# Optimization experiments

Hardware: AMD Instinct MI355X
Metric: run time of the kernel (lower is better)

The kernel has to match this reference:

```python
import jax, jax.numpy as jnp
import numpy as np
from jax import lax

EPS = 1e-5
TRUNK_C, REG_C, GPOOL_C = 256, 192, 64
B, H, W = 256, 19, 19


def setup_inputs() -> dict:
    key = jax.random.key(0)
    ks = jax.random.split(key, 18)
    def bn_params(k, c):
        k1, k2, k3, k4 = jax.random.split(k, 4)
        return (jax.random.normal(k1, (c,)) * 0.1 + 1.0,   # gamma
                jax.random.normal(k2, (c,)) * 0.1,          # beta
                jax.random.normal(k3, (c,)) * 0.1,          # running mean
                jax.random.uniform(k4, (c,)) * 0.5 + 0.5)   # running var
    bn1_g, bn1_b, bn1_m, bn1_v = bn_params(ks[0], TRUNK_C)
    bn1b_g, bn1b_b, bn1b_m, bn1b_v = bn_params(ks[1], GPOOL_C)
    bn2_g, bn2_b, bn2_m, bn2_v = bn_params(ks[2], REG_C)
    x = jax.random.normal(ks[3], (B, TRUNK_C, H, W), dtype=jnp.float32)
    w1a = jax.random.normal(ks[4], (REG_C, TRUNK_C, 3, 3), dtype=jnp.float32) * (1.0 / np.sqrt(TRUNK_C * 9))
    w1b = jax.random.normal(ks[5], (GPOOL_C, TRUNK_C, 3, 3), dtype=jnp.float32) * (1.0 / np.sqrt(TRUNK_C * 9))
    w_lin = jax.random.normal(ks[6], (REG_C, 3 * GPOOL_C), dtype=jnp.float32) * (1.0 / np.sqrt(3 * GPOOL_C))
    w2 = jax.random.normal(ks[7], (TRUNK_C, REG_C, 3, 3), dtype=jnp.float32) * (1.0 / np.sqrt(REG_C * 9))
    return {
        'x': x, 'bn1_g': bn1_g, 'bn1_b': bn1_b, 'bn1_m': bn1_m, 'bn1_v': bn1_v,
        'w1a': w1a, 'w1b': w1b,
        'bn1b_g': bn1b_g, 'bn1b_b': bn1b_b, 'bn1b_m': bn1b_m, 'bn1b_v': bn1b_v,
        'w_lin': w_lin,
        'bn2_g': bn2_g, 'bn2_b': bn2_b, 'bn2_m': bn2_m, 'bn2_v': bn2_v,
        'w2': w2,
    }


def _bn(x, g, b, m, v):
    # inference batchnorm over channel dim of NCHW
    inv = g / jnp.sqrt(v + EPS)
    return (x - m[:, None, None]) * inv[:, None, None] + b[:, None, None]


def _mish(x):
    return x * jnp.tanh(jax.nn.softplus(x))


def _conv(x, w):
    return lax.conv_general_dilated(x, w, (1, 1), 'SAME',
                                    dimension_numbers=('NCHW', 'OIHW', 'NCHW'))


def _kata_gpool(x):
    # x: [B, C, H, W] -> [B, 3C]: mean, mean*(sqrt(N)-14)/10, max
    b, c, h, w = x.shape
    n = float(h * w)
    sqrt_n = n ** 0.5
    mean = jnp.sum(x, axis=(2, 3)) / n
    max_val = jnp.max(x, axis=(2, 3))
    scaled_mean = mean * ((sqrt_n - 14.0) / 10.0)
    return jnp.concatenate([mean, scaled_mean, max_val], axis=1)


def reference(x, bn1_g, bn1_b, bn1_m, bn1_v, w1a, w1b,
              bn1b_g, bn1b_b, bn1b_m, bn1b_v, w_lin,
              bn2_g, bn2_b, bn2_m, bn2_v, w2):
    out = _mish(_bn(x, bn1_g, bn1_b, bn1_m, bn1_v))
    reg = _conv(out, w1a)                       # [B, REG_C, H, W]
    gp = _conv(out, w1b)                        # [B, GPOOL_C, H, W]
    gp = _mish(_bn(gp, bn1b_g, bn1b_b, bn1b_m, bn1b_v))
    gp_pooled = _kata_gpool(gp)                 # [B, 3*GPOOL_C]
    gp_out = gp_pooled @ w_lin.T                # [B, REG_C]
    reg = reg + gp_out[:, :, None, None]
    out2 = _mish(_bn(reg, bn2_g, bn2_b, bn2_m, bn2_v))
    out2 = _conv(out2, w2)
    return out2 + x
```

## Files before the change

kernel.cpp:

```cpp
#include <hip/hip_runtime.h>
#include <hip/hip_bf16.h>
#include <math.h>


#define BATCH   256
#define TRUNK_C 256
#define REG_C   192
#define GPOOL_C 64
#define HH      19
#define WW      19
#define HW      361
#define PP      441
#define EPS     1e-5f

typedef __hip_bfloat16 bf16;
typedef __attribute__((ext_vector_type(8))) short short8;
typedef __attribute__((ext_vector_type(4))) float floatx4;

__device__ __forceinline__ float b2f(bf16 v) { return __bfloat162float(v); }
__device__ __forceinline__ bf16  f2b(float v) { return __float2bfloat16(v); }

__device__ __forceinline__ float mish_f(float v) {
    if (v > 20.0f) return v;
    float u = __expf(v);
    float n = u * (u + 2.0f);
    return v * __fdividef(n, n + 2.0f);
}

__device__ __forceinline__ void gload_lds16(const void* gsrc, void* lds) {
    __builtin_amdgcn_global_load_lds(
        (const __attribute__((address_space(1))) void*)gsrc,
        (__attribute__((address_space(3))) void*)lds, 16, 0, 0);
}

__global__ void prep_bn_kernel(const float* g1, const float* b1, const float* m1, const float* v1,
                               const float* g1b, const float* b1b, const float* m1b, const float* v1b,
                               const float* g2, const float* b2, const float* m2, const float* v2,
                               float* bnbuf) {
    int t = threadIdx.x;
    if (t < 256) {
        float s = g1[t] / sqrtf(v1[t] + EPS);
        bnbuf[t] = s;
        bnbuf[256 + t] = b1[t] - m1[t] * s;
    } else if (t < 320) {
        int c = t - 256;
        float s = g1b[c] / sqrtf(v1b[c] + EPS);
        bnbuf[512 + c] = s;
        bnbuf[576 + c] = b1b[c] - m1b[c] * s;
    } else if (t < 512) {
        int c = t - 320;
        float s = g2[c] / sqrtf(v2[c] + EPS);
        bnbuf[640 + c] = s;
        bnbuf[832 + c] = b2[c] - m2[c] * s;
    }
}

__global__ void prep_w_kernel(const float* __restrict__ w1a, const float* __restrict__ w1b,
                              const float* __restrict__ w2,
                              bf16* __restrict__ w1c_p, bf16* __restrict__ w2_p) {
    const int T1 = 16 * 72 * 64 * 8;
    const int T2 = 16 * 54 * 64 * 8;
    for (int i = blockIdx.x * blockDim.x + threadIdx.x; i < T1 + T2;
         i += gridDim.x * blockDim.x) {
        if (i < T1) {
            int j = i & 7, lane = (i >> 3) & 63;
            int kc = (i >> 9) % 72, cog = (i >> 9) / 72;
            int co = cog * 16 + (lane & 15);
            int k = kc * 32 + ((lane >> 4) << 3) + j;
            int r = k >> 8, ci = k & 255;
            float v = (co < 192) ? w1a[co * 2304 + ci * 9 + r]
                                 : w1b[(co - 192) * 2304 + ci * 9 + r];
            w1c_p[i] = f2b(v);
        } else {
            int i2 = i - T1;
            int j = i2 & 7, lane = (i2 >> 3) & 63;
            int kc = (i2 >> 9) % 54, cog = (i2 >> 9) / 54;
            int co = cog * 16 + (lane & 15);
            int k = kc * 32 + ((lane >> 4) << 3) + j;
            int r = k / 192, ci = k % 192;
            w2_p[i2] = f2b(w2[co * 1728 + ci * 9 + r]);
        }
    }
}

__global__ void zero_border_kernel(bf16* __restrict__ act_pad, bf16* __restrict__ reg_pad) {
    int b = blockIdx.x;
    int t = threadIdx.x;
    for (int pp = 0; pp < PP; ++pp) {
        int r = pp / 21, c = pp % 21;
        bool border = (r == 0) | (r == 20) | (c == 0) | (c == 20);
        if (!border) continue;
        act_pad[((size_t)b * PP + pp) * TRUNK_C + t] = f2b(0.0f);
        if (t < REG_C) reg_pad[((size_t)b * PP + pp) * REG_C + t] = f2b(0.0f);
    }
}

__global__ __launch_bounds__(256)
void bn1_mish_t_kernel(const float* __restrict__ x, const float* __restrict__ bnbuf,
                       bf16* __restrict__ act_pad) {
    __shared__ float lds[256][32];
    int pc = blockIdx.x;
    int b  = blockIdx.y;
    int t  = threadIdx.x;
    int p0 = pc * 32;
    int px = t & 31;
#pragma unroll
    for (int it = 0; it < 32; ++it) {
        int ci = it * 8 + (t >> 5);
        int p  = p0 + px;
        float v = 0.0f;
        if (p < HW) v = x[((size_t)b * TRUNK_C + ci) * HW + p];
        v = v * bnbuf[ci] + bnbuf[256 + ci];
        lds[ci][px ^ (ci >> 3)] = mish_f(v);
    }
    __syncthreads();
#pragma unroll
    for (int it = 0; it < 4; ++it) {
        int pl = it * 8 + (t >> 5);
        int p  = p0 + pl;
        if (p >= HW) continue;
        int ch = t & 31;
        short8 vv;
#pragma unroll
        for (int j = 0; j < 8; ++j) {
            bf16 h = f2b(lds[ch * 8 + j][pl ^ ch]);
            short s;
            __builtin_memcpy(&s, &h, 2);
            vv[j] = s;
        }
        int pp = (p / WW + 1) * 21 + (p % WW + 1);
        *(short8*)(act_pad + ((size_t)b * PP + pp) * TRUNK_C + ch * 8) = vv;
    }
}

__global__ __launch_bounds__(512)
void conv1_kernel(const bf16* __restrict__ act,
                  const bf16* __restrict__ wfrag,
                  bf16* __restrict__ reg_out,
                  bf16* __restrict__ gp_out,
                  const float* __restrict__ ep_scale, const float* __restrict__ ep_bias) {
    const int CIN = 256, NKC = 72;
    __shared__ __align__(16) bf16 atile[3][128 * 32];
    const int b   = blockIdx.x;
    const int mt  = blockIdx.y;
    const int t   = threadIdx.x;
    const int w   = t >> 6, lane = t & 63;
    const int mi  = w >> 2, ni = w & 3;
    const int l15 = lane & 15, quad = lane >> 4;

    int spxl = t >> 2;
    int sq   = t & 3;
    int ss   = sq ^ ((spxl >> 1) & 3);
    int sp   = mt * 128 + spxl; if (sp > 360) sp = 360;
    const bf16* sbase = act + ((size_t)b * PP + (sp / WW) * 21 + (sp % WW)) * CIN + (ss << 3);

    const bf16* wb[4];
#pragma unroll
    for (int ns = 0; ns < 4; ++ns)
        wb[ns] = wfrag + ((size_t)(ni * 4 + ns) * NKC * 64 + lane) * 8;

    int aoff[4];
#pragma unroll
    for (int ms = 0; ms < 4; ++ms) {
        int row = mi * 64 + ms * 16 + l15;
        aoff[ms] = row * 32 + ((quad ^ ((row >> 1) & 3)) << 3);
    }

    auto stage = [&](int buf, int kc) {
        int r = kc >> 3, c = kc & 7;
        int off = ((r / 3) * 21 + (r % 3)) * CIN + (c << 5);
        gload_lds16(sbase + off, &atile[buf][w << 9]);
    };

    floatx4 acc[4][4];
#pragma unroll
    for (int i = 0; i < 4; ++i)
#pragma unroll
        for (int j = 0; j < 4; ++j) acc[i][j] = (floatx4){0.f, 0.f, 0.f, 0.f};

    short8 afr[4], bfrA[4], bfrB[4];
    stage(0, 0);
    stage(1, 1);
#pragma unroll
    for (int ns = 0; ns < 4; ++ns) bfrA[ns] = *(const short8*)(wb[ns]);

    for (int kc = 0; kc < NKC; kc += 2) {
        asm volatile("s_waitcnt vmcnt(5)" ::: "memory");
        __builtin_amdgcn_sched_barrier(0);
        __builtin_amdgcn_s_barrier();
        __builtin_amdgcn_sched_barrier(0);
        {
            int s1 = kc + 2; if (s1 > NKC - 1) s1 = NKC - 1;
            stage((kc + 2) % 3, s1);
        }
#pragma unroll
        for (int ns = 0; ns < 4; ++ns)
            bfrB[ns] = *(const short8*)(wb[ns] + (size_t)(kc + 1) * 512);
        {
            const bf16* at = atile[kc % 3];
#pragma unroll
            for (int ms = 0; ms < 4; ++ms)
                afr[ms] = *(const short8*)(at + aoff[ms]);
        }
#pragma unroll
        for (int ms = 0; ms < 4; ++ms)
#pragma unroll
            for (int ns = 0; ns < 4; ++ns)
                acc[ms][ns] = __builtin_amdgcn_mfma_f32_16x16x32_bf16(
                    afr[ms], bfrA[ns], acc[ms][ns], 0, 0, 0);

        asm volatile("s_waitcnt vmcnt(5)" ::: "memory");
        __builtin_amdgcn_sched_barrier(0);
        __builtin_amdgcn_s_barrier();
        __builtin_amdgcn_sched_barrier(0);
        {
            int s2 = kc + 3; if (s2 > NKC - 1) s2 = NKC - 1;
            stage((kc + 3) % 3, s2);
        }
        {
            int nb = kc + 2; if (nb > NKC - 1) nb = NKC - 1;
#pragma unroll
            for (int ns = 0; ns < 4; ++ns)
                bfrA[ns] = *(const short8*)(wb[ns] + (size_t)nb * 512);
        }
        {
            const bf16* at = atile[(kc + 1) % 3];
#pragma unroll
            for (int ms = 0; ms < 4; ++ms)
                afr[ms] = *(const short8*)(at + aoff[ms]);
        }
#pragma unroll
        for (int ms = 0; ms < 4; ++ms)
#pragma unroll
            for (int ns = 0; ns < 4; ++ns)
                acc[ms][ns] = __builtin_amdgcn_mfma_f32_16x16x32_bf16(
                    afr[ms], bfrB[ns], acc[ms][ns], 0, 0, 0);
    }

    float scl[4], bia[4];
#pragma unroll
    for (int ns = 0; ns < 4; ++ns) {
        int co = (ni * 4 + ns) * 16 + l15;
        if (co >= 192) { scl[ns] = ep_scale[co - 192]; bia[ns] = ep_bias[co - 192]; }
    }
#pragma unroll
    for (int ms = 0; ms < 4; ++ms) {
#pragma unroll
        for (int rg = 0; rg < 4; ++rg) {
            int p = mt * 128 + mi * 64 + ms * 16 + quad * 4 + rg;
            if (p > 360) continue;
            size_t ppad = (size_t)b * PP + (p / WW + 1) * 21 + (p % WW + 1);
#pragma unroll
            for (int ns = 0; ns < 4; ++ns) {
                int co = (ni * 4 + ns) * 16 + l15;
                float v = acc[ms][ns][rg];
                if (co < 192) {
                    reg_out[ppad * REG_C + co] = f2b(v);
                } else {
                    v = mish_f(v * scl[ns] + bia[ns]);
                    gp_out[((size_t)b * HW + p) * GPOOL_C + (co - 192)] = f2b(v);
                }
            }
        }
    }
}

__global__ __launch_bounds__(512)
void conv2_kernel(const bf16* __restrict__ act,
                  const bf16* __restrict__ wfrag,
                  const float* __restrict__ resid,
                  float* __restrict__ out) {
    const int CIN = 192, NKC = 54;
    __shared__ __align__(16) bf16 atile[3][128 * 32];
    const int b   = blockIdx.x;
    const int mt  = blockIdx.y;
    const int t   = threadIdx.x;
    const int w   = t >> 6, lane = t & 63;
    const int pw  = w >> 2, cw = w & 3;
    const int l15 = lane & 15, quad = lane >> 4;

    int spxl = t >> 2;
    int sq   = t & 3;
    int ss   = sq ^ ((spxl >> 1) & 3);
    int sp   = mt * 128 + spxl; if (sp > 360) sp = 360;
    const bf16* sbase = act + ((size_t)b * PP + (sp / WW) * 21 + (sp % WW)) * CIN + (ss << 3);

    const bf16* wb[4];
#pragma unroll
    for (int ms = 0; ms < 4; ++ms)
        wb[ms] = wfrag + ((size_t)(cw * 4 + ms) * NKC * 64 + lane) * 8;

    int aoff[4];
#pragma unroll
    for (int ns = 0; ns < 4; ++ns) {
        int row = pw * 64 + ns * 16 + l15;
        aoff[ns] = row * 32 + ((quad ^ ((row >> 1) & 3)) << 3);
    }

    auto stage = [&](int buf, int kc) {
        int r = kc / 6, c = kc % 6;
        int off = ((r / 3) * 21 + (r % 3)) * CIN + (c << 5);
        gload_lds16(sbase + off, &atile[buf][w << 9]);
    };

    floatx4 acc[4][4];
#pragma unroll
    for (int i = 0; i < 4; ++i)
#pragma unroll
        for (int j = 0; j < 4; ++j) acc[i][j] = (floatx4){0.f, 0.f, 0.f, 0.f};

    short8 bfa[4], wfrA[4], wfrB[4];
    stage(0, 0);
    stage(1, 1);
#pragma unroll
    for (int ms = 0; ms < 4; ++ms) wfrA[ms] = *(const short8*)(wb[ms]);

    for (int kc = 0; kc < NKC; kc += 2) {
        asm volatile("s_waitcnt vmcnt(5)" ::: "memory");
        __builtin_amdgcn_sched_barrier(0);
        __builtin_amdgcn_s_barrier();
        __builtin_amdgcn_sched_barrier(0);
        {
            int s1 = kc + 2; if (s1 > NKC - 1) s1 = NKC - 1;
            stage((kc + 2) % 3, s1);
        }
#pragma unroll
        for (int ms = 0; ms < 4; ++ms)
            wfrB[ms] = *(const short8*)(wb[ms] + (size_t)(kc + 1) * 512);
        {
            const bf16* at = atile[kc % 3];
#pragma unroll
            for (int ns = 0; ns < 4; ++ns)
                bfa[ns] = *(const short8*)(at + aoff[ns]);
        }
#pragma unroll
        for (int ms = 0; ms < 4; ++ms)
#pragma unroll
            for (int ns = 0; ns < 4; ++ns)
                acc[ms][ns] = __builtin_amdgcn_mfma_f32_16x16x32_bf16(
                    wfrA[ms], bfa[ns], acc[ms][ns], 0, 0, 0);

        asm volatile("s_waitcnt vmcnt(5)" ::: "memory");
        __builtin_amdgcn_sched_barrier(0);
        __builtin_amdgcn_s_barrier();
        __builtin_amdgcn_sched_barrier(0);
        {
            int s2 = kc + 3; if (s2 > NKC - 1) s2 = NKC - 1;
            stage((kc + 3) % 3, s2);
        }
        {
            int nb = kc + 2; if (nb > NKC - 1) nb = NKC - 1;
#pragma unroll
            for (int ms = 0; ms < 4; ++ms)
                wfrA[ms] = *(const short8*)(wb[ms] + (size_t)nb * 512);
        }
        {
            const bf16* at = atile[(kc + 1) % 3];
#pragma unroll
            for (int ns = 0; ns < 4; ++ns)
                bfa[ns] = *(const short8*)(at + aoff[ns]);
        }
#pragma unroll
        for (int ms = 0; ms < 4; ++ms)
#pragma unroll
            for (int ns = 0; ns < 4; ++ns)
                acc[ms][ns] = __builtin_amdgcn_mfma_f32_16x16x32_bf16(
                    wfrB[ms], bfa[ns], acc[ms][ns], 0, 0, 0);
    }

#pragma unroll
    for (int ns = 0; ns < 4; ++ns) {
        int p = mt * 128 + pw * 64 + ns * 16 + l15;
        if (p > 360) continue;
#pragma unroll
        for (int ms = 0; ms < 4; ++ms) {
#pragma unroll
            for (int rg = 0; rg < 4; ++rg) {
                int co = (cw * 4 + ms) * 16 + quad * 4 + rg;
                size_t idx = ((size_t)b * TRUNK_C + co) * HW + p;
                out[idx] = acc[ms][ns][rg] + resid[idx];
            }
        }
    }
}

__global__ void gpool_lin_kernel(const bf16* __restrict__ gp, const float* __restrict__ w_lin,
                                 float* __restrict__ gpout) {
    __shared__ float ls[4][64], lm[4][64];
    __shared__ float pooled_s[192];
    int b = blockIdx.x;
    int t = threadIdx.x;
    int c = t & 63, sub = t >> 6;
    float s = 0.0f, mx = -1e30f;
    for (int p = sub; p < HW; p += 4) {
        float v = b2f(gp[((size_t)b * HW + p) * GPOOL_C + c]);
        s += v;
        mx = fmaxf(mx, v);
    }
    ls[sub][c] = s; lm[sub][c] = mx;
    __syncthreads();
    if (t < 64) {
        float ss = ls[0][t] + ls[1][t] + ls[2][t] + ls[3][t];
        float mm = fmaxf(fmaxf(lm[0][t], lm[1][t]), fmaxf(lm[2][t], lm[3][t]));
        float mean = ss * (1.0f / 361.0f);
        pooled_s[t] = mean;
        pooled_s[64 + t] = mean * 0.5f;
        pooled_s[128 + t] = mm;
    }
    __syncthreads();
    if (t < 192) {
        const float4* wr4 = (const float4*)(w_lin + t * 192);
        float acc = 0.0f;
#pragma unroll 8
        for (int j = 0; j < 48; ++j) {
            float4 wv = wr4[j];
            acc = fmaf(pooled_s[j * 4 + 0], wv.x, acc);
            acc = fmaf(pooled_s[j * 4 + 1], wv.y, acc);
            acc = fmaf(pooled_s[j * 4 + 2], wv.z, acc);
            acc = fmaf(pooled_s[j * 4 + 3], wv.w, acc);
        }
        gpout[b * 192 + t] = acc;
    }
}

__global__ __launch_bounds__(256)
void add_bn2_mish_kernel(bf16* __restrict__ reg_pad, const float* __restrict__ gpout,
                         const float* __restrict__ bnbuf) {
    const int total = BATCH * HW * 24;
    int i = blockIdx.x * blockDim.x + threadIdx.x;
    if (i >= total) return;
    int g  = i % 24;
    int bp = i / 24;
    int p  = bp % HW;
    int b  = bp / HW;
    int pp = (p / WW + 1) * 21 + (p % WW + 1);
    size_t idx = ((size_t)b * PP + pp) * REG_C + g * 8;
    short8 v = *(const short8*)(reg_pad + idx);
    const float* gpo = gpout + b * 192 + g * 8;
    const float* sc  = bnbuf + 640 + g * 8;
    const float* bi  = bnbuf + 832 + g * 8;
    short8 o;
#pragma unroll
    for (int j = 0; j < 8; ++j) {
        short sj = v[j];
        bf16 h;
        __builtin_memcpy(&h, &sj, 2);
        float f = b2f(h) + gpo[j];
        f = f * sc[j] + bi[j];
        h = f2b(mish_f(f));
        __builtin_memcpy(&sj, &h, 2);
        o[j] = sj;
    }
    *(short8*)(reg_pad + idx) = o;
}

extern "C" void kernel_launch(void* const* d_in, const int* in_sizes, int n_in,
                              void* d_out, int out_size, void* d_ws, size_t ws_size,
                              hipStream_t stream) {
    const float* x     = (const float*)d_in[0];
    const float* bn1_g = (const float*)d_in[1];
    const float* bn1_b = (const float*)d_in[2];
    const float* bn1_m = (const float*)d_in[3];
    const float* bn1_v = (const float*)d_in[4];
    const float* w1a   = (const float*)d_in[5];
    const float* w1b   = (const float*)d_in[6];
    const float* bn1b_g = (const float*)d_in[7];
    const float* bn1b_b = (const float*)d_in[8];
    const float* bn1b_m = (const float*)d_in[9];
    const float* bn1b_v = (const float*)d_in[10];
    const float* w_lin  = (const float*)d_in[11];
    const float* bn2_g  = (const float*)d_in[12];
    const float* bn2_b  = (const float*)d_in[13];
    const float* bn2_m  = (const float*)d_in[14];
    const float* bn2_v  = (const float*)d_in[15];
    const float* w2     = (const float*)d_in[16];
    float* out = (float*)d_out;

    char* ws = (char*)d_ws;
    size_t off = 0;
    auto alloc = [&](size_t bytes) {
        void* p = ws + off;
        off += (bytes + 255) & ~(size_t)255;
        return p;
    };
    bf16*  act_pad = (bf16*)alloc((size_t)BATCH * PP * TRUNK_C * sizeof(bf16));
    bf16*  reg_pad = (bf16*)alloc((size_t)BATCH * PP * REG_C * sizeof(bf16));
    bf16*  gp      = (bf16*)alloc((size_t)BATCH * HW * GPOOL_C * sizeof(bf16));
    bf16*  w1c_p   = (bf16*)alloc((size_t)16 * 72 * 64 * 8 * sizeof(bf16));
    bf16*  w2_p    = (bf16*)alloc((size_t)16 * 54 * 64 * 8 * sizeof(bf16));
    float* gpout   = (float*)alloc((size_t)BATCH * 192 * sizeof(float));
    float* bnbuf   = (float*)alloc(1024 * sizeof(float));
    (void)ws_size;

    hipLaunchKernelGGL(prep_bn_kernel, dim3(1), dim3(512), 0, stream,
                       bn1_g, bn1_b, bn1_m, bn1_v,
                       bn1b_g, bn1b_b, bn1b_m, bn1b_v,
                       bn2_g, bn2_b, bn2_m, bn2_v, bnbuf);
    hipLaunchKernelGGL(prep_w_kernel, dim3(1024), dim3(256), 0, stream,
                       w1a, w1b, w2, w1c_p, w2_p);
    hipLaunchKernelGGL(zero_border_kernel, dim3(BATCH), dim3(256), 0, stream,
                       act_pad, reg_pad);

    hipLaunchKernelGGL(bn1_mish_t_kernel, dim3(12, BATCH), dim3(256), 0, stream,
                       x, bnbuf, act_pad);

    hipLaunchKernelGGL(conv1_kernel, dim3(BATCH, 3), dim3(512), 0, stream,
                       act_pad, w1c_p, reg_pad, gp, bnbuf + 512, bnbuf + 576);

    hipLaunchKernelGGL(gpool_lin_kernel, dim3(BATCH), dim3(256), 0, stream,
                       gp, w_lin, gpout);

    {
        int total = BATCH * HW * 24;
        hipLaunchKernelGGL(add_bn2_mish_kernel, dim3((total + 255) / 256), dim3(256), 0, stream,
                           reg_pad, gpout, bnbuf);
    }

    hipLaunchKernelGGL(conv2_kernel, dim3(BATCH, 3), dim3(512), 0, stream,
                       reg_pad, w2_p, x, out);
}
```

Before: 680.8 us.

## Split conv output channels across grid z, deepen LDS pipeline, merge prep kernels

Both conv kernels now use 256-thread blocks with a third grid dimension that splits output channels in two, so each block computes half the channels for its 128-pixel tile. The LDS A-tile ring grows from three to four buffers and is staged one iteration further ahead, with adjusted vmcnt waits. The three setup kernels (BN folding, weight packing, border zeroing) are merged into one flat launch, and border zeroing becomes vectorized. This adds more concurrent blocks and deeper latency hiding, at the cost of loading each activation tile twice, once per channel half.

```diff
diff --git a/kernel.cpp b/kernel.cpp
--- a/kernel.cpp
+++ b/kernel.cpp
@@ -33,35 +33,23 @@
         (__attribute__((address_space(3))) void*)lds, 16, 0, 0);
 }
 
-__global__ void prep_bn_kernel(const float* g1, const float* b1, const float* m1, const float* v1,
-                               const float* g1b, const float* b1b, const float* m1b, const float* v1b,
-                               const float* g2, const float* b2, const float* m2, const float* v2,
-                               float* bnbuf) {
-    int t = threadIdx.x;
-    if (t < 256) {
-        float s = g1[t] / sqrtf(v1[t] + EPS);
-        bnbuf[t] = s;
-        bnbuf[256 + t] = b1[t] - m1[t] * s;
-    } else if (t < 320) {
-        int c = t - 256;
-        float s = g1b[c] / sqrtf(v1b[c] + EPS);
-        bnbuf[512 + c] = s;
-        bnbuf[576 + c] = b1b[c] - m1b[c] * s;
-    } else if (t < 512) {
-        int c = t - 320;
-        float s = g2[c] / sqrtf(v2[c] + EPS);
-        bnbuf[640 + c] = s;
-        bnbuf[832 + c] = b2[c] - m2[c] * s;
-    }
-}
-
-__global__ void prep_w_kernel(const float* __restrict__ w1a, const float* __restrict__ w1b,
-                              const float* __restrict__ w2,
-                              bf16* __restrict__ w1c_p, bf16* __restrict__ w2_p) {
-    const int T1 = 16 * 72 * 64 * 8;
-    const int T2 = 16 * 54 * 64 * 8;
-    for (int i = blockIdx.x * blockDim.x + threadIdx.x; i < T1 + T2;
-         i += gridDim.x * blockDim.x) {
+__global__ void prep_kernel(
+    const float* g1, const float* b1, const float* m1, const float* v1,
+    const float* g1b, const float* b1b, const float* m1b, const float* v1b,
+    const float* g2, const float* b2, const float* m2, const float* v2,
+    const float* __restrict__ w1a, const float* __restrict__ w1b,
+    const float* __restrict__ w2,
+    bf16* __restrict__ w1c_p, bf16* __restrict__ w2_p,
+    bf16* __restrict__ act_pad, bf16* __restrict__ reg_pad,
+    float* bnbuf)
+{
+    const int T1  = 16 * 72 * 64 * 8;
+    const int T2  = 16 * 54 * 64 * 8;
+    const int TW  = T1 + T2;
+    const int TBa = BATCH * 80 * 32;
+    const int TBr = BATCH * 80 * 24;
+    int i = blockIdx.x * blockDim.x + threadIdx.x;
+    if (i < TW) {
         if (i < T1) {
             int j = i & 7, lane = (i >> 3) & 63;
             int kc = (i >> 9) % 72, cog = (i >> 9) / 72;
@@ -80,18 +68,39 @@
             int r = k / 192, ci = k % 192;
             w2_p[i2] = f2b(w2[co * 1728 + ci * 9 + r]);
         }
-    }
-}
-
-__global__ void zero_border_kernel(bf16* __restrict__ act_pad, bf16* __restrict__ reg_pad) {
-    int b = blockIdx.x;
-    int t = threadIdx.x;
-    for (int pp = 0; pp < PP; ++pp) {
-        int r = pp / 21, c = pp % 21;
-        bool border = (r == 0) | (r == 20) | (c == 0) | (c == 20);
-        if (!border) continue;
-        act_pad[((size_t)b * PP + pp) * TRUNK_C + t] = f2b(0.0f);
-        if (t < REG_C) reg_pad[((size_t)b * PP + pp) * REG_C + t] = f2b(0.0f);
+    } else if (i < TW + TBa + TBr) {
+        int j = i - TW;
+        bool isact = j < TBa;
+        if (!isact) j -= TBa;
+        int nb = isact ? 32 : 24;
+        int b = j / (80 * nb);
+        int rem = j - b * (80 * nb);
+        int e = rem / nb, g = rem - (rem / nb) * nb;
+        int pp;
+        if (e < 21) pp = e;
+        else if (e < 42) pp = 420 + (e - 21);
+        else if (e < 61) pp = (e - 41) * 21;
+        else pp = (e - 60) * 21 + 20;
+        short8 z = {0, 0, 0, 0, 0, 0, 0, 0};
+        if (isact) *(short8*)(act_pad + ((size_t)b * PP + pp) * TRUNK_C + g * 8) = z;
+        else       *(short8*)(reg_pad + ((size_t)b * PP + pp) * REG_C + g * 8) = z;
+    } else {
+        int t = i - (TW + TBa + TBr);
+        if (t < 256) {
+            float s = g1[t] / sqrtf(v1[t] + EPS);
+            bnbuf[t] = s;
+            bnbuf[256 + t] = b1[t] - m1[t] * s;
+        } else if (t < 320) {
+            int c = t - 256;
+            float s = g1b[c] / sqrtf(v1b[c] + EPS);
+            bnbuf[512 + c] = s;
+            bnbuf[576 + c] = b1b[c] - m1b[c] * s;
+        } else if (t < 512) {
+            int c = t - 320;
+            float s = g2[c] / sqrtf(v2[c] + EPS);
+            bnbuf[640 + c] = s;
+            bnbuf[832 + c] = b2[c] - m2[c] * s;
+        }
     }
 }
 
@@ -133,31 +142,34 @@
     }
 }
 
-__global__ __launch_bounds__(512)
+__global__ __launch_bounds__(256, 3)
 void conv1_kernel(const bf16* __restrict__ act,
                   const bf16* __restrict__ wfrag,
                   bf16* __restrict__ reg_out,
                   bf16* __restrict__ gp_out,
                   const float* __restrict__ ep_scale, const float* __restrict__ ep_bias) {
     const int CIN = 256, NKC = 72;
-    __shared__ __align__(16) bf16 atile[3][128 * 32];
+    __shared__ __align__(16) bf16 atile[4][128 * 32];
     const int b   = blockIdx.x;
     const int mt  = blockIdx.y;
+    const int nh  = blockIdx.z;
     const int t   = threadIdx.x;
     const int w   = t >> 6, lane = t & 63;
-    const int mi  = w >> 2, ni = w & 3;
+    const int mi  = w >> 1, ni = w & 1;
     const int l15 = lane & 15, quad = lane >> 4;
 
-    int spxl = t >> 2;
+    int row0 = t >> 2;
     int sq   = t & 3;
-    int ss   = sq ^ ((spxl >> 1) & 3);
-    int sp   = mt * 128 + spxl; if (sp > 360) sp = 360;
-    const bf16* sbase = act + ((size_t)b * PP + (sp / WW) * 21 + (sp % WW)) * CIN + (ss << 3);
+    int ss   = sq ^ ((row0 >> 1) & 3);
+    int sp0  = mt * 128 + row0;      if (sp0 > 360) sp0 = 360;
+    int sp1  = mt * 128 + row0 + 64; if (sp1 > 360) sp1 = 360;
+    const bf16* sb0 = act + ((size_t)b * PP + (sp0 / WW) * 21 + (sp0 % WW)) * CIN + (ss << 3);
+    const bf16* sb1 = act + ((size_t)b * PP + (sp1 / WW) * 21 + (sp1 % WW)) * CIN + (ss << 3);
 
     const bf16* wb[4];
 #pragma unroll
     for (int ns = 0; ns < 4; ++ns)
-        wb[ns] = wfrag + ((size_t)(ni * 4 + ns) * NKC * 64 + lane) * 8;
+        wb[ns] = wfrag + ((size_t)(nh * 8 + ni * 4 + ns) * NKC * 64 + lane) * 8;
 
     int aoff[4];
 #pragma unroll
@@ -169,7 +181,9 @@
     auto stage = [&](int buf, int kc) {
         int r = kc >> 3, c = kc & 7;
         int off = ((r / 3) * 21 + (r % 3)) * CIN + (c << 5);
-        gload_lds16(sbase + off, &atile[buf][w << 9]);
+        bf16* dst = &atile[buf][w << 9];
+        gload_lds16(sb0 + off, dst);
+        gload_lds16(sb1 + off, dst + 2048);
     };
 
     floatx4 acc[4][4];
@@ -181,23 +195,28 @@
     short8 afr[4], bfrA[4], bfrB[4];
     stage(0, 0);
     stage(1, 1);
+    asm volatile("" ::: "memory");
 #pragma unroll
     for (int ns = 0; ns < 4; ++ns) bfrA[ns] = *(const short8*)(wb[ns]);
+    asm volatile("" ::: "memory");
+    stage(2, 2);
 
     for (int kc = 0; kc < NKC; kc += 2) {
-        asm volatile("s_waitcnt vmcnt(5)" ::: "memory");
+        if (kc == 0) asm volatile("s_waitcnt vmcnt(8)" ::: "memory");
+        else         asm volatile("s_waitcnt vmcnt(12)" ::: "memory");
         __builtin_amdgcn_sched_barrier(0);
         __builtin_amdgcn_s_barrier();
         __builtin_amdgcn_sched_barrier(0);
-        {
-            int s1 = kc + 2; if (s1 > NKC - 1) s1 = NKC - 1;
-            stage((kc + 2) % 3, s1);
-        }
 #pragma unroll
         for (int ns = 0; ns < 4; ++ns)
             bfrB[ns] = *(const short8*)(wb[ns] + (size_t)(kc + 1) * 512);
-        {
-            const bf16* at = atile[kc % 3];
+        asm volatile("" ::: "memory");
+        {
+            int s = kc + 3; if (s > NKC - 1) s = NKC - 1;
+            stage((kc + 3) & 3, s);
+        }
+        {
+            const bf16* at = atile[kc & 3];
 #pragma unroll
             for (int ms = 0; ms < 4; ++ms)
                 afr[ms] = *(const short8*)(at + aoff[ms]);
@@ -209,22 +228,23 @@
                 acc[ms][ns] = __builtin_amdgcn_mfma_f32_16x16x32_bf16(
                     afr[ms], bfrA[ns], acc[ms][ns], 0, 0, 0);
 
-        asm volatile("s_waitcnt vmcnt(5)" ::: "memory");
+        asm volatile("s_waitcnt vmcnt(12)" ::: "memory");
         __builtin_amdgcn_sched_barrier(0);
         __builtin_amdgcn_s_barrier();
         __builtin_amdgcn_sched_barrier(0);
         {
-            int s2 = kc + 3; if (s2 > NKC - 1) s2 = NKC - 1;
-            stage((kc + 3) % 3, s2);
-        }
-        {
             int nb = kc + 2; if (nb > NKC - 1) nb = NKC - 1;
 #pragma unroll
             for (int ns = 0; ns < 4; ++ns)
                 bfrA[ns] = *(const short8*)(wb[ns] + (size_t)nb * 512);
         }
-        {
-            const bf16* at = atile[(kc + 1) % 3];
+        asm volatile("" ::: "memory");
+        {
+            int s = kc + 4; if (s > NKC - 1) s = NKC - 1;
+            stage((kc + 4) & 3, s);
+        }
+        {
+            const bf16* at = atile[(kc + 1) & 3];
 #pragma unroll
             for (int ms = 0; ms < 4; ++ms)
                 afr[ms] = *(const short8*)(at + aoff[ms]);
@@ -240,7 +260,7 @@
     float scl[4], bia[4];
 #pragma unroll
     for (int ns = 0; ns < 4; ++ns) {
-        int co = (ni * 4 + ns) * 16 + l15;
+        int co = (nh * 8 + ni * 4 + ns) * 16 + l15;
         if (co >= 192) { scl[ns] = ep_scale[co - 192]; bia[ns] = ep_bias[co - 192]; }
     }
 #pragma unroll
@@ -252,7 +272,7 @@
             size_t ppad = (size_t)b * PP + (p / WW + 1) * 21 + (p % WW + 1);
 #pragma unroll
             for (int ns = 0; ns < 4; ++ns) {
-                int co = (ni * 4 + ns) * 16 + l15;
+                int co = (nh * 8 + ni * 4 + ns) * 16 + l15;
                 float v = acc[ms][ns][rg];
                 if (co < 192) {
                     reg_out[ppad * REG_C + co] = f2b(v);
@@ -265,30 +285,33 @@
     }
 }
 
-__global__ __launch_bounds__(512)
+__global__ __launch_bounds__(256, 3)
 void conv2_kernel(const bf16* __restrict__ act,
                   const bf16* __restrict__ wfrag,
                   const float* __restrict__ resid,
                   float* __restrict__ out) {
     const int CIN = 192, NKC = 54;
-    __shared__ __align__(16) bf16 atile[3][128 * 32];
+    __shared__ __align__(16) bf16 atile[4][128 * 32];
     const int b   = blockIdx.x;
     const int mt  = blockIdx.y;
+    const int nh  = blockIdx.z;
     const int t   = threadIdx.x;
     const int w   = t >> 6, lane = t & 63;
-    const int pw  = w >> 2, cw = w & 3;
+    const int pw  = w >> 1, cw = w & 1;
     const int l15 = lane & 15, quad = lane >> 4;
 
-    int spxl = t >> 2;
+    int row0 = t >> 2;
     int sq   = t & 3;
-    int ss   = sq ^ ((spxl >> 1) & 3);
-    int sp   = mt * 128 + spxl; if (sp > 360) sp = 360;
-    const bf16* sbase = act + ((size_t)b * PP + (sp / WW) * 21 + (sp % WW)) * CIN + (ss << 3);
+    int ss   = sq ^ ((row0 >> 1) & 3);
+    int sp0  = mt * 128 + row0;      if (sp0 > 360) sp0 = 360;
+    int sp1  = mt * 128 + row0 + 64; if (sp1 > 360) sp1 = 360;
+    const bf16* sb0 = act + ((size_t)b * PP + (sp0 / WW) * 21 + (sp0 % WW)) * CIN + (ss << 3);
+    const bf16* sb1 = act + ((size_t)b * PP + (sp1 / WW) * 21 + (sp1 % WW)) * CIN + (ss << 3);
 
     const bf16* wb[4];
 #pragma unroll
     for (int ms = 0; ms < 4; ++ms)
-        wb[ms] = wfrag + ((size_t)(cw * 4 + ms) * NKC * 64 + lane) * 8;
+        wb[ms] = wfrag + ((size_t)(nh * 8 + cw * 4 + ms) * NKC * 64 + lane) * 8;
 
     int aoff[4];
 #pragma unroll
@@ -300,7 +323,9 @@
     auto stage = [&](int buf, int kc) {
         int r = kc / 6, c = kc % 6;
         int off = ((r / 3) * 21 + (r % 3)) * CIN + (c << 5);
-        gload_lds16(sbase + off, &atile[buf][w << 9]);
+        bf16* dst = &atile[buf][w << 9];
+        gload_lds16(sb0 + off, dst);
+        gload_lds16(sb1 + off, dst + 2048);
     };
 
     floatx4 acc[4][4];
@@ -312,23 +337,28 @@
     short8 bfa[4], wfrA[4], wfrB[4];
     stage(0, 0);
     stage(1, 1);
+    asm volatile("" ::: "memory");
 #pragma unroll
     for (int ms = 0; ms < 4; ++ms) wfrA[ms] = *(const short8*)(wb[ms]);
+    asm volatile("" ::: "memory");
+    stage(2, 2);
 
     for (int kc = 0; kc < NKC; kc += 2) {
-        asm volatile("s_waitcnt vmcnt(5)" ::: "memory");
+        if (kc == 0) asm volatile("s_waitcnt vmcnt(8)" ::: "memory");
+        else         asm volatile("s_waitcnt vmcnt(12)" ::: "memory");
         __builtin_amdgcn_sched_barrier(0);
         __builtin_amdgcn_s_barrier();
         __builtin_amdgcn_sched_barrier(0);
-        {
-            int s1 = kc + 2; if (s1 > NKC - 1) s1 = NKC - 1;
-            stage((kc + 2) % 3, s1);
-        }
 #pragma unroll
         for (int ms = 0; ms < 4; ++ms)
             wfrB[ms] = *(const short8*)(wb[ms] + (size_t)(kc + 1) * 512);
-        {
-            const bf16* at = atile[kc % 3];
+        asm volatile("" ::: "memory");
+        {
+            int s = kc + 3; if (s > NKC - 1) s = NKC - 1;
+            stage((kc + 3) & 3, s);
+        }
+        {
+            const bf16* at = atile[kc & 3];
 #pragma unroll
             for (int ns = 0; ns < 4; ++ns)
                 bfa[ns] = *(const short8*)(at + aoff[ns]);
@@ -340,22 +370,23 @@
                 acc[ms][ns] = __builtin_amdgcn_mfma_f32_16x16x32_bf16(
                     wfrA[ms], bfa[ns], acc[ms][ns], 0, 0, 0);
 
-        asm volatile("s_waitcnt vmcnt(5)" ::: "memory");
+        asm volatile("s_waitcnt vmcnt(12)" ::: "memory");
         __builtin_amdgcn_sched_barrier(0);
         __builtin_amdgcn_s_barrier();
         __builtin_amdgcn_sched_barrier(0);
-        {
-            int s2 = kc + 3; if (s2 > NKC - 1) s2 = NKC - 1;
-            stage((kc + 3) % 3, s2);
-        }
         {
             int nb = kc + 2; if (nb > NKC - 1) nb = NKC - 1;
 #pragma unroll
             for (int ms = 0; ms < 4; ++ms)
                 wfrA[ms] = *(const short8*)(wb[ms] + (size_t)nb * 512);
         }
-        {
-            const bf16* at = atile[(kc + 1) % 3];
+        asm volatile("" ::: "memory");
+        {
+            int s = kc + 4; if (s > NKC - 1) s = NKC - 1;
+            stage((kc + 4) & 3, s);
+        }
+        {
+            const bf16* at = atile[(kc + 1) & 3];
 #pragma unroll
             for (int ns = 0; ns < 4; ++ns)
                 bfa[ns] = *(const short8*)(at + aoff[ns]);
@@ -376,7 +407,7 @@
         for (int ms = 0; ms < 4; ++ms) {
 #pragma unroll
             for (int rg = 0; rg < 4; ++rg) {
-                int co = (cw * 4 + ms) * 16 + quad * 4 + rg;
+                int co = (nh * 8 + cw * 4 + ms) * 16 + quad * 4 + rg;
                 size_t idx = ((size_t)b * TRUNK_C + co) * HW + p;
                 out[idx] = acc[ms][ns][rg] + resid[idx];
             }
@@ -492,19 +523,20 @@
     float* bnbuf   = (float*)alloc(1024 * sizeof(float));
     (void)ws_size;
 
-    hipLaunchKernelGGL(prep_bn_kernel, dim3(1), dim3(512), 0, stream,
-                       bn1_g, bn1_b, bn1_m, bn1_v,
-                       bn1b_g, bn1b_b, bn1b_m, bn1b_v,
-                       bn2_g, bn2_b, bn2_m, bn2_v, bnbuf);
-    hipLaunchKernelGGL(prep_w_kernel, dim3(1024), dim3(256), 0, stream,
-                       w1a, w1b, w2, w1c_p, w2_p);
-    hipLaunchKernelGGL(zero_border_kernel, dim3(BATCH), dim3(256), 0, stream,
-                       act_pad, reg_pad);
+    {
+        const int total = (16 * 72 * 64 * 8) + (16 * 54 * 64 * 8)
+                        + BATCH * 80 * 32 + BATCH * 80 * 24 + 512;
+        hipLaunchKernelGGL(prep_kernel, dim3((total + 255) / 256), dim3(256), 0, stream,
+                           bn1_g, bn1_b, bn1_m, bn1_v,
+                           bn1b_g, bn1b_b, bn1b_m, bn1b_v,
+                           bn2_g, bn2_b, bn2_m, bn2_v,
+                           w1a, w1b, w2, w1c_p, w2_p, act_pad, reg_pad, bnbuf);
+    }
 
     hipLaunchKernelGGL(bn1_mish_t_kernel, dim3(12, BATCH), dim3(256), 0, stream,
                        x, bnbuf, act_pad);
 
-    hipLaunchKernelGGL(conv1_kernel, dim3(BATCH, 3), dim3(512), 0, stream,
+    hipLaunchKernelGGL(conv1_kernel, dim3(BATCH, 3, 2), dim3(256), 0, stream,
                        act_pad, w1c_p, reg_pad, gp, bnbuf + 512, bnbuf + 576);
 
     hipLaunchKernelGGL(gpool_lin_kernel, dim3(BATCH), dim3(256), 0, stream,
@@ -516,6 +548,6 @@
                            reg_pad, gpout, bnbuf);
     }
 
-    hipLaunchKernelGGL(conv2_kernel, dim3(BATCH, 3), dim3(512), 0, stream,
+    hipLaunchKernelGGL(conv2_kernel, dim3(BATCH, 3, 2), dim3(256), 0, stream,
                        reg_pad, w2_p, x, out);
 }
```

After: 669.2 us. No clear change (-1.7%).
